# Kernel tuning notes

Hardware: AMD Instinct MI355X
Metric: run time of the kernel (lower is better)

Reference implementation:

```python
import jax, jax.numpy as jnp
import numpy as np

B_, L_, DIN, DM, DS, DR, K = 2, 1024, 1024, 2048, 16, 128, 4


def setup_inputs() -> dict:
    key = jax.random.key(0)
    ks = jax.random.split(key, 10)
    s = lambda k, shape, sc=0.02: (jax.random.normal(k, shape, jnp.float32) * sc)
    A_init = jnp.tile(jnp.arange(1, DS + 1, dtype=jnp.float32)[None, :], (DM, 1))  # (DM, DS)
    return {
        'x_in': jax.random.normal(ks[0], (B_, L_, DIN), jnp.float32),
        'W_in': s(ks[1], (DIN, DM)),
        'W_res': s(ks[2], (DIN, DM)),
        'W_out': s(ks[3], (DM, DIN)),
        'conv_w': s(ks[4], (DM, K), 0.1),   # depthwise conv weight (torch shape (DM,1,K) squeezed)
        'conv_b': jnp.zeros((DM,), jnp.float32),
        'A_log': jnp.log(A_init),
        'D': jnp.ones((DM,), jnp.float32),
        'W_B': s(ks[5], (DM, DS)),
        'W_C': s(ks[6], (DM, DS)),
        'W_dt': s(ks[7], (DM, DR)),
        'dt_w': s(ks[8], (DR, DM)),
        'dt_b': jnp.zeros((DM,), jnp.float32),
    }


def reference(x_in, W_in, W_res, W_out, conv_w, conv_b, A_log, D, W_B, W_C, W_dt, dt_w, dt_b):
    Bb, L, _ = x_in.shape
    x = x_in @ W_in                     # (B, L, DM)
    res = x_in @ W_res                  # (B, L, DM)
    # Causal depthwise conv1d: pad left k-1, truncate to L (matches Conv1d(padding=k-1)[:, :, :L])
    xp = jnp.pad(x, ((0, 0), (K - 1, 0), (0, 0)))
    xc = conv_b
    for i in range(K):
        xc = xc + xp[:, i:i + L, :] * conv_w[:, i]
    xc = jax.nn.silu(xc)                # (B, L, DM)
    # Selective SSM (fused_ssm)
    A = -jnp.exp(A_log)                 # (DM, DS)
    Bp = xc @ W_B                       # (B, L, DS)
    Cp = xc @ W_C                       # (B, L, DS)
    delta = jax.nn.softplus((xc @ W_dt) @ dt_w + dt_b)  # (B, L, DM)
    dA = jnp.exp(delta[..., None] * A)                       # (B, L, DM, DS)
    dBu = delta[..., None] * Bp[:, :, None, :] * xc[..., None]  # (B, L, DM, DS)

    def step(h, inp):
        dA_t, dBu_t, C_t = inp
        h = dA_t * h + dBu_t                         # (B, DM, DS)
        y = jnp.einsum('bdn,bn->bd', h, C_t)         # (B, DM)
        return h, y

    h0 = jnp.zeros((Bb, DM, DS), jnp.float32)
    _, ys = jax.lax.scan(step, h0, (dA.transpose(1, 0, 2, 3), dBu.transpose(1, 0, 2, 3), Cp.transpose(1, 0, 2)))
    y = ys.transpose(1, 0, 2) + D * xc  # (B, L, DM)
    y = y * jax.nn.silu(res)
    return y @ W_out                    # (B, L, DIN)
```

## Files before the change

### kernel.cpp

```cpp
#include <hip/hip_runtime.h>
#include <hip/hip_bf16.h>

constexpr int B_  = 2;
constexpr int L_  = 1024;
constexpr int DIN = 1024;
constexpr int DM  = 2048;
constexpr int DS  = 16;
constexpr int DR  = 128;
constexpr int KC  = 4;
constexpr int M_  = B_ * L_;
constexpr int NP2 = 256;
constexpr int NPC = 160;
constexpr int KSLICES = 8;
constexpr int KSL = DM / KSLICES;

constexpr int NC = 32;
constexpr int CL = L_ / NC;
constexpr int S_ = B_ * DM * DS;

typedef __bf16 bf16x8 __attribute__((ext_vector_type(8)));
typedef float  f32x4  __attribute__((ext_vector_type(4)));

__device__ __forceinline__ void gload_lds16(const void* g, void* l) {
    __builtin_amdgcn_global_load_lds(
        (const __attribute__((address_space(1))) void*)g,
        (__attribute__((address_space(3))) void*)l, 16, 0, 0);
}

__device__ __forceinline__ void transpose_block(const float* __restrict__ in,
                                                __bf16* __restrict__ out,
                                                int R, int C, int bx, int by, int t) {
    __shared__ float tile[32][33];
    int tx = t & 31, ty = t >> 5;
    #pragma unroll
    for (int j = 0; j < 32; j += 8)
        tile[ty + j][tx] = in[(size_t)(by * 32 + ty + j) * C + (bx * 32 + tx)];
    __syncthreads();
    #pragma unroll
    for (int j = 0; j < 32; j += 8)
        out[(size_t)(bx * 32 + ty + j) * R + (by * 32 + tx)] = (__bf16)tile[tx][ty + j];
}

__global__ void prep_all(const float* __restrict__ x_in, const float* __restrict__ W_in,
                         const float* __restrict__ W_res, const float* __restrict__ W_out,
                         const float* __restrict__ dt_w,
                         const float* __restrict__ W_B, const float* __restrict__ W_C,
                         const float* __restrict__ W_dt, const float* __restrict__ conv_w,
                         __bf16* __restrict__ xinB, __bf16* __restrict__ WinT,
                         __bf16* __restrict__ WresT, __bf16* __restrict__ WoutT,
                         __bf16* __restrict__ dtwT, __bf16* __restrict__ projW,
                         float* __restrict__ cwT) {
    int blk = blockIdx.x, t = threadIdx.x;
    if (blk < 8192) {
        int i = blk * 256 + t;
        xinB[i] = (__bf16)x_in[i];
    } else if (blk < 10240) {
        int b = blk - 8192;
        transpose_block(W_in, WinT, DIN, DM, b % 64, b / 64, t);
    } else if (blk < 12288) {
        int b = blk - 10240;
        transpose_block(W_res, WresT, DIN, DM, b % 64, b / 64, t);
    } else if (blk < 14336) {
        int b = blk - 12288;
        transpose_block(W_out, WoutT, DM, DIN, b % 32, b / 32, t);
    } else if (blk < 14592) {
        int b = blk - 14336;
        transpose_block(dt_w, dtwT, DR, DM, b % 64, b / 64, t);
    } else if (blk < 16640) {
        int i = (blk - 14592) * 256 + t;
        int k = i % DM;
        int n = i / DM;
        float v = 0.f;
        if (n < 16)        v = W_B[(size_t)k * DS + n];
        else if (n < 32)   v = W_C[(size_t)k * DS + (n - 16)];
        else if (n < 160)  v = W_dt[(size_t)k * DR + (n - 32)];
        projW[i] = (__bf16)v;
    } else {
        int j = (blk - 16640) * 256 + t;
        int tap = j / DM, d = j % DM;
        cwT[j] = conv_w[d * KC + tap];
    }
}

__global__ void reduce_split(const __bf16* __restrict__ PpartB, float* __restrict__ Bp,
                             float* __restrict__ Cp, __bf16* __restrict__ dtmpB) {
    int i = blockIdx.x * 256 + threadIdx.x;
    int row = i / NPC, c = i % NPC;
    float v = 0.f;
    #pragma unroll
    for (int ks = 0; ks < KSLICES; ks++)
        v += (float)PpartB[(size_t)ks * M_ * NPC + i];
    if (c < 16)       Bp[(size_t)row * DS + c] = v;
    else if (c < 32)  Cp[(size_t)row * DS + (c - 16)] = v;
    else              dtmpB[(size_t)row * DR + (c - 32)] = (__bf16)v;
}

template<int EPI>
__global__ void gemm_tile128(const __bf16* __restrict__ A, const __bf16* __restrict__ BT,
                             float* __restrict__ Cf, __bf16* __restrict__ Cb,
                             const float* __restrict__ bias, int M, int N, int K,
                             int lda, int ldb) {
    __shared__ __bf16 sA[2][128 * 32];
    __shared__ __bf16 sB[2][128 * 32];
    int t = threadIdx.x;
    int lane = t & 63, w = t >> 6;
    int wm = w >> 1, wn = w & 1;
    int m0 = blockIdx.y * 128, n0 = blockIdx.x * 128;
    int kbase = blockIdx.z * K;
    int q = lane >> 4, rr = lane & 15;

    f32x4 acc[4][4] = {};

    int srow = t >> 2;
    int slot = t & 3;

    const int nt = K >> 5;

    #pragma unroll
    for (int rnd = 0; rnd < 2; rnd++) {
        int row = srow + rnd * 64;
        int gkb = slot ^ ((row >> 1) & 3);
        gload_lds16(A  + (size_t)(m0 + row) * lda + kbase + gkb * 8,
                    &sA[0][rnd * 2048 + w * 512]);
        gload_lds16(BT + (size_t)(n0 + row) * ldb + kbase + gkb * 8,
                    &sB[0][rnd * 2048 + w * 512]);
    }
    __syncthreads();

    int cur = 0;
    for (int tix = 0; tix < nt; tix++) {
        if (tix + 1 < nt) {
            int kt = (tix + 1) << 5;
            #pragma unroll
            for (int rnd = 0; rnd < 2; rnd++) {
                int row = srow + rnd * 64;
                int gkb = slot ^ ((row >> 1) & 3);
                gload_lds16(A  + (size_t)(m0 + row) * lda + kbase + kt + gkb * 8,
                            &sA[cur ^ 1][rnd * 2048 + w * 512]);
                gload_lds16(BT + (size_t)(n0 + row) * ldb + kbase + kt + gkb * 8,
                            &sB[cur ^ 1][rnd * 2048 + w * 512]);
            }
        }

        bf16x8 af[4], bfr[4];
        #pragma unroll
        for (int i = 0; i < 4; i++) {
            int rowA = wm * 64 + i * 16 + rr;
            af[i] = *(const bf16x8*)(&sA[cur][rowA * 32 + ((q ^ ((rowA >> 1) & 3)) * 8)]);
            int rowB = wn * 64 + i * 16 + rr;
            bfr[i] = *(const bf16x8*)(&sB[cur][rowB * 32 + ((q ^ ((rowB >> 1) & 3)) * 8)]);
        }
        #pragma unroll
        for (int i = 0; i < 4; i++)
            #pragma unroll
            for (int j = 0; j < 4; j++)
                acc[i][j] = __builtin_amdgcn_mfma_f32_16x16x32_bf16(af[i], bfr[j], acc[i][j], 0, 0, 0);

        __syncthreads();
        cur ^= 1;
    }

    #pragma unroll
    for (int i = 0; i < 4; i++) {
        #pragma unroll
        for (int j = 0; j < 4; j++) {
            int col = n0 + wn * 64 + j * 16 + rr;
            #pragma unroll
            for (int jj = 0; jj < 4; jj++) {
                int row = m0 + wm * 64 + i * 16 + q * 4 + jj;
                float v = acc[i][j][jj];
                if (EPI == 1) {
                    float z = v + bias[col];
                    Cb[(size_t)row * N + col] = (__bf16)((z > 20.f) ? z : log1pf(__expf(z)));
                } else if (EPI == 2) {
                    if (col < DM) ((__bf16*)Cf)[(size_t)row * DM + col] = (__bf16)v;
                    else          Cb[(size_t)row * DM + (col - DM)] = (__bf16)v;
                } else {
                    if (col < NPC)
                        Cb[(size_t)blockIdx.z * M * NPC + (size_t)row * NPC + col] = (__bf16)v;
                }
            }
        }
    }
}

__global__ void gemm_out64(const __bf16* __restrict__ A, const __bf16* __restrict__ BT,
                           float* __restrict__ C, int M, int N, int K, int lda, int ldb) {
    __shared__ __bf16 sA[2][128 * 32];
    __shared__ __bf16 sB[2][64 * 32];
    int t = threadIdx.x;
    int lane = t & 63, w = t >> 6;
    int m0 = blockIdx.y * 128, n0 = blockIdx.x * 64;
    int q = lane >> 4, rr = lane & 15;

    f32x4 acc[2][4] = {};
    int srow = t >> 2;
    int slot = t & 3;

    const int nt = K >> 5;

    {
        #pragma unroll
        for (int rnd = 0; rnd < 2; rnd++) {
            int row = srow + rnd * 64;
            int gkb = slot ^ ((row >> 1) & 3);
            gload_lds16(A + (size_t)(m0 + row) * lda + gkb * 8,
                        &sA[0][rnd * 2048 + w * 512]);
        }
        int gkb = slot ^ ((srow >> 1) & 3);
        gload_lds16(BT + (size_t)(n0 + srow) * ldb + gkb * 8,
                    &sB[0][w * 512]);
    }
    __syncthreads();

    int cur = 0;
    for (int tix = 0; tix < nt; tix++) {
        if (tix + 1 < nt) {
            int kt = (tix + 1) << 5;
            #pragma unroll
            for (int rnd = 0; rnd < 2; rnd++) {
                int row = srow + rnd * 64;
                int gkb = slot ^ ((row >> 1) & 3);
                gload_lds16(A + (size_t)(m0 + row) * lda + kt + gkb * 8,
                            &sA[cur ^ 1][rnd * 2048 + w * 512]);
            }
            int gkb = slot ^ ((srow >> 1) & 3);
            gload_lds16(BT + (size_t)(n0 + srow) * ldb + kt + gkb * 8,
                        &sB[cur ^ 1][w * 512]);
        }

        bf16x8 af[2], bfr[4];
        #pragma unroll
        for (int i = 0; i < 2; i++) {
            int rowA = w * 32 + i * 16 + rr;
            af[i] = *(const bf16x8*)(&sA[cur][rowA * 32 + ((q ^ ((rowA >> 1) & 3)) * 8)]);
        }
        #pragma unroll
        for (int j = 0; j < 4; j++) {
            int rowB = j * 16 + rr;
            bfr[j] = *(const bf16x8*)(&sB[cur][rowB * 32 + ((q ^ ((rowB >> 1) & 3)) * 8)]);
        }
        #pragma unroll
        for (int i = 0; i < 2; i++)
            #pragma unroll
            for (int j = 0; j < 4; j++)
                acc[i][j] = __builtin_amdgcn_mfma_f32_16x16x32_bf16(af[i], bfr[j], acc[i][j], 0, 0, 0);

        __syncthreads();
        cur ^= 1;
    }

    #pragma unroll
    for (int i = 0; i < 2; i++) {
        #pragma unroll
        for (int j = 0; j < 4; j++) {
            int col = n0 + j * 16 + rr;
            #pragma unroll
            for (int jj = 0; jj < 4; jj++) {
                int row = m0 + w * 32 + i * 16 + q * 4 + jj;
                C[(size_t)row * N + col] = acc[i][j][jj];
            }
        }
    }
}

__global__ void conv_silu(const __bf16* __restrict__ x, const float* __restrict__ cwT,
                          const float* __restrict__ bias, __bf16* __restrict__ xcB) {
    int row = blockIdx.x;
    int d   = threadIdx.x * 8;
    int l   = row % L_;
    size_t base = (size_t)row * DM + d;

    float acc[8];
    {
        const f32x4* b4 = (const f32x4*)(bias + d);
        f32x4 b0 = b4[0], b1 = b4[1];
        #pragma unroll
        for (int q = 0; q < 4; q++) { acc[q] = b0[q]; acc[4 + q] = b1[q]; }
    }
    #pragma unroll
    for (int i = 0; i < KC; i++) {
        int li = l - (KC - 1) + i;
        if (li >= 0) {
            bf16x8 xv = *(const bf16x8*)(x + base + (size_t)(i - (KC - 1)) * DM);
            const f32x4* w4 = (const f32x4*)(cwT + (size_t)i * DM + d);
            f32x4 w0 = w4[0], w1 = w4[1];
            #pragma unroll
            for (int q = 0; q < 4; q++) {
                acc[q]     = fmaf((float)xv[q],     w0[q], acc[q]);
                acc[4 + q] = fmaf((float)xv[4 + q], w1[q], acc[4 + q]);
            }
        }
    }
    bf16x8 out;
    #pragma unroll
    for (int q = 0; q < 8; q++) {
        float v = acc[q] / (1.f + __expf(-acc[q]));
        out[q] = (__bf16)v;
    }
    *(bf16x8*)(xcB + base) = out;
}

__global__ void scan_phase1(const __bf16* __restrict__ delta, const __bf16* __restrict__ xc,
                            const float* __restrict__ Bp, const float* __restrict__ A_log,
                            __bf16* __restrict__ aprodB, __bf16* __restrict__ cendB) {
    int blk = blockIdx.x;
    int c   = blk % NC;
    int rem = blk / NC;
    int dmt = rem % (DM / 256);
    int b   = rem / (DM / 256);
    int t   = threadIdx.x;
    int dm  = dmt * 256 + t;
    int l0  = c * CL;

    __shared__ float sB[CL * DS];
    sB[t]       = Bp[((size_t)b * L_ + l0) * DS + t];
    sB[t + 256] = Bp[((size_t)b * L_ + l0) * DS + t + 256];
    __syncthreads();

    float Aval[DS];
    {
        const f32x4* Ap = (const f32x4*)(A_log + (size_t)dm * DS);
        #pragma unroll
        for (int r4 = 0; r4 < 4; r4++) {
            f32x4 a = Ap[r4];
            #pragma unroll
            for (int q = 0; q < 4; q++) Aval[r4 * 4 + q] = -__expf(a[q]);
        }
    }

    float h[DS], ap[DS];
    #pragma unroll
    for (int i = 0; i < DS; i++) { h[i] = 0.f; ap[i] = 1.f; }

    size_t base = ((size_t)b * L_ + l0) * DM + dm;
    #pragma unroll 4
    for (int j = 0; j < CL; j++) {
        float dl  = (float)delta[base + (size_t)j * DM];
        float xv  = (float)xc[base + (size_t)j * DM];
        float cmn = dl * xv;
        const f32x4* sB4 = (const f32x4*)(sB + j * DS);
        #pragma unroll
        for (int r4 = 0; r4 < 4; r4++) {
            f32x4 bv = sB4[r4];
            #pragma unroll
            for (int q = 0; q < 4; q++) {
                int i = r4 * 4 + q;
                float dA = __expf(dl * Aval[i]);
                ap[i] *= dA;
                h[i] = fmaf(dA, h[i], cmn * bv[q]);
            }
        }
    }

    size_t s = ((size_t)(b * DM + dm)) * DS;
    #pragma unroll
    for (int r8 = 0; r8 < 2; r8++) {
        bf16x8 va, vh;
        #pragma unroll
        for (int q = 0; q < 8; q++) { va[q] = (__bf16)ap[r8 * 8 + q]; vh[q] = (__bf16)h[r8 * 8 + q]; }
        ((bf16x8*)(aprodB + (size_t)c * S_ + s))[r8] = va;
        ((bf16x8*)(cendB  + (size_t)c * S_ + s))[r8] = vh;
    }
}

__global__ void scan_phase2(const __bf16* __restrict__ aprodB, const __bf16* __restrict__ cendB,
                            __bf16* __restrict__ hinitB) {
    int u = blockIdx.x * 256 + threadIdx.x;
    float h = 0.f;
    #pragma unroll
    for (int c = 0; c < NC; c++) {
        float a  = (float)aprodB[(size_t)c * S_ + u];
        float ce = (float)cendB [(size_t)c * S_ + u];
        hinitB[(size_t)c * S_ + u] = (__bf16)h;
        h = fmaf(a, h, ce);
    }
}

__global__ void scan_phase3(const __bf16* __restrict__ delta, const __bf16* __restrict__ xc,
                            const float* __restrict__ Bp, const float* __restrict__ Cp,
                            const __bf16* __restrict__ res, const float* __restrict__ A_log,
                            const float* __restrict__ Dw, const __bf16* __restrict__ hinitB,
                            __bf16* __restrict__ ybar) {
    int blk = blockIdx.x;
    int c   = blk % NC;
    int rem = blk / NC;
    int dmt = rem % (DM / 256);
    int b   = rem / (DM / 256);
    int t   = threadIdx.x;
    int dm  = dmt * 256 + t;
    int l0  = c * CL;

    __shared__ float sB[CL * DS];
    __shared__ float sC[CL * DS];
    sB[t]       = Bp[((size_t)b * L_ + l0) * DS + t];
    sB[t + 256] = Bp[((size_t)b * L_ + l0) * DS + t + 256];
    sC[t]       = Cp[((size_t)b * L_ + l0) * DS + t];
    sC[t + 256] = Cp[((size_t)b * L_ + l0) * DS + t + 256];
    __syncthreads();

    float Aval[DS];
    {
        const f32x4* Ap = (const f32x4*)(A_log + (size_t)dm * DS);
        #pragma unroll
        for (int r4 = 0; r4 < 4; r4++) {
            f32x4 a = Ap[r4];
            #pragma unroll
            for (int q = 0; q < 4; q++) Aval[r4 * 4 + q] = -__expf(a[q]);
        }
    }
    float Dval = Dw[dm];

    float h[DS];
    {
        size_t s = ((size_t)(b * DM + dm)) * DS;
        #pragma unroll
        for (int r8 = 0; r8 < 2; r8++) {
            bf16x8 v = ((const bf16x8*)(hinitB + (size_t)c * S_ + s))[r8];
            #pragma unroll
            for (int q = 0; q < 8; q++) h[r8 * 8 + q] = (float)v[q];
        }
    }

    size_t base = ((size_t)b * L_ + l0) * DM + dm;
    #pragma unroll 4
    for (int j = 0; j < CL; j++) {
        float dl  = (float)delta[base + (size_t)j * DM];
        float xv  = (float)xc[base + (size_t)j * DM];
        float rv  = (float)res[base + (size_t)j * DM];
        float cmn = dl * xv;
        float y = 0.f;
        const f32x4* sB4 = (const f32x4*)(sB + j * DS);
        const f32x4* sC4 = (const f32x4*)(sC + j * DS);
        #pragma unroll
        for (int r4 = 0; r4 < 4; r4++) {
            f32x4 bv = sB4[r4];
            f32x4 cv = sC4[r4];
            #pragma unroll
            for (int q = 0; q < 4; q++) {
                int i = r4 * 4 + q;
                float dA = __expf(dl * Aval[i]);
                h[i] = fmaf(dA, h[i], cmn * bv[q]);
                y = fmaf(h[i], cv[q], y);
            }
        }
        float g = rv / (1.f + __expf(-rv));
        ybar[base + (size_t)j * DM] = (__bf16)((y + Dval * xv) * g);
    }
}

extern "C" void kernel_launch(void* const* d_in, const int* in_sizes, int n_in,
                              void* d_out, int out_size, void* d_ws, size_t ws_size,
                              hipStream_t stream) {
    const float* x_in   = (const float*)d_in[0];
    const float* W_in   = (const float*)d_in[1];
    const float* W_res  = (const float*)d_in[2];
    const float* W_out  = (const float*)d_in[3];
    const float* conv_w = (const float*)d_in[4];
    const float* conv_b = (const float*)d_in[5];
    const float* A_log  = (const float*)d_in[6];
    const float* Dw     = (const float*)d_in[7];
    const float* W_B    = (const float*)d_in[8];
    const float* W_C    = (const float*)d_in[9];
    const float* W_dt   = (const float*)d_in[10];
    const float* dt_w   = (const float*)d_in[11];
    const float* dt_b   = (const float*)d_in[12];

    float* ws_f = (float*)d_ws;
    float* Bp    = ws_f;
    float* Cp    = Bp + (size_t)M_ * DS;
    float* cwT   = Cp + (size_t)M_ * DS;
    __bf16* bf_base = (__bf16*)(cwT + (size_t)KC * DM);
    __bf16* ybar   = bf_base;
    __bf16* xinB   = ybar   + (size_t)M_ * DM;
    __bf16* WinT   = xinB   + (size_t)M_ * DIN;
    __bf16* WresT  = WinT   + (size_t)DM * DIN;
    __bf16* WoutT  = WresT  + (size_t)DM * DIN;
    __bf16* xB     = WoutT  + (size_t)DIN * DM;
    __bf16* xcB    = xB     + (size_t)M_ * DM;
    __bf16* projW  = xcB    + (size_t)M_ * DM;
    __bf16* dtwT   = projW  + (size_t)NP2 * DM;
    __bf16* dtmpB  = dtwT   + (size_t)DM * DR;
    __bf16* deltaB = dtmpB  + (size_t)M_ * DR;
    __bf16* resB   = deltaB + (size_t)M_ * DM;
    __bf16* aprodB = resB   + (size_t)M_ * DM;
    __bf16* cendB  = aprodB + (size_t)NC * S_;
    __bf16* hinitB = cendB  + (size_t)NC * S_;
    __bf16* PpartB = hinitB + (size_t)NC * S_;

    prep_all<<<16672, 256, 0, stream>>>(x_in, W_in, W_res, W_out, dt_w, W_B, W_C, W_dt,
                                        conv_w, xinB, WinT, WresT, WoutT, dtwT, projW, cwT);

    gemm_tile128<2><<<dim3((2 * DM) / 128, M_ / 128, 1), 256, 0, stream>>>(
        xinB, WinT, (float*)xB, resB, nullptr, M_, 2 * DM, DIN, DIN, DIN);

    conv_silu<<<M_, 256, 0, stream>>>(xB, cwT, conv_b, xcB);

    gemm_tile128<4><<<dim3(NP2 / 128, M_ / 128, KSLICES), 256, 0, stream>>>(
        xcB, projW, nullptr, PpartB, nullptr, M_, NP2, KSL, DM, DM);
    reduce_split<<<(M_ * NPC) / 256, 256, 0, stream>>>(PpartB, Bp, Cp, dtmpB);

    gemm_tile128<1><<<dim3(DM / 128, M_ / 128, 1), 256, 0, stream>>>(
        dtmpB, dtwT, nullptr, deltaB, dt_b, M_, DM, DR, DR, DR);

    int nblk = B_ * (DM / 256) * NC;
    scan_phase1<<<nblk, 256, 0, stream>>>(deltaB, xcB, Bp, A_log, aprodB, cendB);
    scan_phase2<<<S_ / 256, 256, 0, stream>>>(aprodB, cendB, hinitB);
    scan_phase3<<<nblk, 256, 0, stream>>>(deltaB, xcB, Bp, Cp, resB, A_log, Dw, hinitB, ybar);

    gemm_out64<<<dim3(DIN / 64, M_ / 128), 256, 0, stream>>>(
        ybar, WoutT, (float*)d_out, M_, DIN, DM, DM, DM);
}
```

Measured before the change: 263.3 us.

## Triple-buffer GEMM LDS tiles with explicit vmcnt waits and raw barriers

Both bf16 GEMM kernels move from double to triple buffering of the LDS tiles. Two tiles are prefetched ahead via global_load_lds, and each wait uses explicit s_waitcnt vmcnt counts with raw s_barrier instead of __syncthreads. The aim is to hide more global-load latency behind the MFMA work. In exchange LDS use grows by half, which may lower occupancy. The hand-counted vmcnt values are fragile if the compiler issues other vector memory ops, and raw barriers do not wait on LDS reads the way __syncthreads does.

```diff
diff --git a/kernel.cpp b/kernel.cpp
--- a/kernel.cpp
+++ b/kernel.cpp
@@ -26,6 +26,8 @@
         (const __attribute__((address_space(1))) void*)g,
         (__attribute__((address_space(3))) void*)l, 16, 0, 0);
 }
+
+#define VMCNT(N) asm volatile("s_waitcnt vmcnt(" #N ")" ::: "memory")
 
 __device__ __forceinline__ void transpose_block(const float* __restrict__ in,
                                                 __bf16* __restrict__ out,
@@ -100,8 +102,8 @@
                              float* __restrict__ Cf, __bf16* __restrict__ Cb,
                              const float* __restrict__ bias, int M, int N, int K,
                              int lda, int ldb) {
-    __shared__ __bf16 sA[2][128 * 32];
-    __shared__ __bf16 sB[2][128 * 32];
+    __shared__ __bf16 sA[3][128 * 32];
+    __shared__ __bf16 sB[3][128 * 32];
     int t = threadIdx.x;
     int lane = t & 63, w = t >> 6;
     int wm = w >> 1, wn = w & 1;
@@ -116,32 +118,29 @@
 
     const int nt = K >> 5;
 
-    #pragma unroll
-    for (int rnd = 0; rnd < 2; rnd++) {
-        int row = srow + rnd * 64;
-        int gkb = slot ^ ((row >> 1) & 3);
-        gload_lds16(A  + (size_t)(m0 + row) * lda + kbase + gkb * 8,
-                    &sA[0][rnd * 2048 + w * 512]);
-        gload_lds16(BT + (size_t)(n0 + row) * ldb + kbase + gkb * 8,
-                    &sB[0][rnd * 2048 + w * 512]);
-    }
-    __syncthreads();
+    auto stage = [&](int tile, int bufi) {
+        int kt = tile << 5;
+        #pragma unroll
+        for (int rnd = 0; rnd < 2; rnd++) {
+            int row = srow + rnd * 64;
+            int gkb = slot ^ ((row >> 1) & 3);
+            gload_lds16(A  + (size_t)(m0 + row) * lda + kbase + kt + gkb * 8,
+                        &sA[bufi][rnd * 2048 + w * 512]);
+            gload_lds16(BT + (size_t)(n0 + row) * ldb + kbase + kt + gkb * 8,
+                        &sB[bufi][rnd * 2048 + w * 512]);
+        }
+    };
+
+    if (0 < nt) stage(0, 0);
+    if (1 < nt) stage(1, 1);
+    if (2 < nt) stage(2, 2);
+    if (nt >= 3)      { VMCNT(8); }
+    else if (nt == 2) { VMCNT(4); }
+    else              { VMCNT(0); }
+    __builtin_amdgcn_s_barrier();
 
     int cur = 0;
     for (int tix = 0; tix < nt; tix++) {
-        if (tix + 1 < nt) {
-            int kt = (tix + 1) << 5;
-            #pragma unroll
-            for (int rnd = 0; rnd < 2; rnd++) {
-                int row = srow + rnd * 64;
-                int gkb = slot ^ ((row >> 1) & 3);
-                gload_lds16(A  + (size_t)(m0 + row) * lda + kbase + kt + gkb * 8,
-                            &sA[cur ^ 1][rnd * 2048 + w * 512]);
-                gload_lds16(BT + (size_t)(n0 + row) * ldb + kbase + kt + gkb * 8,
-                            &sB[cur ^ 1][rnd * 2048 + w * 512]);
-            }
-        }
-
         bf16x8 af[4], bfr[4];
         #pragma unroll
         for (int i = 0; i < 4; i++) {
@@ -156,8 +155,16 @@
             for (int j = 0; j < 4; j++)
                 acc[i][j] = __builtin_amdgcn_mfma_f32_16x16x32_bf16(af[i], bfr[j], acc[i][j], 0, 0, 0);
 
-        __syncthreads();
-        cur ^= 1;
+        __builtin_amdgcn_s_barrier();
+        if (tix + 3 < nt) stage(tix + 3, cur);
+        int rem = nt - 1 - tix;
+        if (rem > 0) {
+            if (rem >= 3)      { VMCNT(8); }
+            else if (rem == 2) { VMCNT(4); }
+            else               { VMCNT(0); }
+            __builtin_amdgcn_s_barrier();
+        }
+        cur = (cur == 2) ? 0 : cur + 1;
     }
 
     #pragma unroll
@@ -186,8 +193,8 @@
 
 __global__ void gemm_out64(const __bf16* __restrict__ A, const __bf16* __restrict__ BT,
                            float* __restrict__ C, int M, int N, int K, int lda, int ldb) {
-    __shared__ __bf16 sA[2][128 * 32];
-    __shared__ __bf16 sB[2][64 * 32];
+    __shared__ __bf16 sA[3][128 * 32];
+    __shared__ __bf16 sB[3][64 * 32];
     int t = threadIdx.x;
     int lane = t & 63, w = t >> 6;
     int m0 = blockIdx.y * 128, n0 = blockIdx.x * 64;
@@ -199,36 +206,30 @@
 
     const int nt = K >> 5;
 
-    {
+    auto stage = [&](int tile, int bufi) {
+        int kt = tile << 5;
         #pragma unroll
         for (int rnd = 0; rnd < 2; rnd++) {
             int row = srow + rnd * 64;
             int gkb = slot ^ ((row >> 1) & 3);
-            gload_lds16(A + (size_t)(m0 + row) * lda + gkb * 8,
-                        &sA[0][rnd * 2048 + w * 512]);
+            gload_lds16(A + (size_t)(m0 + row) * lda + kt + gkb * 8,
+                        &sA[bufi][rnd * 2048 + w * 512]);
         }
         int gkb = slot ^ ((srow >> 1) & 3);
-        gload_lds16(BT + (size_t)(n0 + srow) * ldb + gkb * 8,
-                    &sB[0][w * 512]);
-    }
-    __syncthreads();
+        gload_lds16(BT + (size_t)(n0 + srow) * ldb + kt + gkb * 8,
+                    &sB[bufi][w * 512]);
+    };
+
+    if (0 < nt) stage(0, 0);
+    if (1 < nt) stage(1, 1);
+    if (2 < nt) stage(2, 2);
+    if (nt >= 3)      { VMCNT(6); }
+    else if (nt == 2) { VMCNT(3); }
+    else              { VMCNT(0); }
+    __builtin_amdgcn_s_barrier();
 
     int cur = 0;
     for (int tix = 0; tix < nt; tix++) {
-        if (tix + 1 < nt) {
-            int kt = (tix + 1) << 5;
-            #pragma unroll
-            for (int rnd = 0; rnd < 2; rnd++) {
-                int row = srow + rnd * 64;
-                int gkb = slot ^ ((row >> 1) & 3);
-                gload_lds16(A + (size_t)(m0 + row) * lda + kt + gkb * 8,
-                            &sA[cur ^ 1][rnd * 2048 + w * 512]);
-            }
-            int gkb = slot ^ ((srow >> 1) & 3);
-            gload_lds16(BT + (size_t)(n0 + srow) * ldb + kt + gkb * 8,
-                        &sB[cur ^ 1][w * 512]);
-        }
-
         bf16x8 af[2], bfr[4];
         #pragma unroll
         for (int i = 0; i < 2; i++) {
@@ -246,8 +247,16 @@
             for (int j = 0; j < 4; j++)
                 acc[i][j] = __builtin_amdgcn_mfma_f32_16x16x32_bf16(af[i], bfr[j], acc[i][j], 0, 0, 0);
 
-        __syncthreads();
-        cur ^= 1;
+        __builtin_amdgcn_s_barrier();
+        if (tix + 3 < nt) stage(tix + 3, cur);
+        int rem = nt - 1 - tix;
+        if (rem > 0) {
+            if (rem >= 3)      { VMCNT(6); }
+            else if (rem == 2) { VMCNT(3); }
+            else               { VMCNT(0); }
+            __builtin_amdgcn_s_barrier();
+        }
+        cur = (cur == 2) ? 0 : cur + 1;
     }
 
     #pragma unroll
```

After: 375.1 us. 42.4% more time.

## Use 8 waves per block in GEMM kernels with smaller per-wave subtiles

Applied to the files above, without the earlier changes.

All bf16 MFMA GEMM kernels are launched with 512 threads instead of 256. The block tile stays the same, but each wave now owns half as many output fragments: 64x32 instead of 64x64 in the 128x128 kernel, and 32x32 instead of 32x64 in the output GEMM. The LDS staging is restructured so each thread issues one async global-to-LDS load per matrix per k-step, and the B load in the 64-wide kernel is guarded to threads below 256. The aim is more waves per CU for latency hiding and fewer accumulator registers per thread. In exchange, each wave reuses fragments less, which means more LDS reads per MFMA, and larger blocks add barrier cost.

```diff
diff --git a/kernel.cpp b/kernel.cpp
--- a/kernel.cpp
+++ b/kernel.cpp
@@ -104,56 +104,48 @@
     __shared__ __bf16 sB[2][128 * 32];
     int t = threadIdx.x;
     int lane = t & 63, w = t >> 6;
-    int wm = w >> 1, wn = w & 1;
+    int wm = w >> 2, wn = w & 3;
     int m0 = blockIdx.y * 128, n0 = blockIdx.x * 128;
     int kbase = blockIdx.z * K;
     int q = lane >> 4, rr = lane & 15;
 
-    f32x4 acc[4][4] = {};
+    f32x4 acc[4][2] = {};
 
     int srow = t >> 2;
     int slot = t & 3;
 
     const int nt = K >> 5;
 
-    #pragma unroll
-    for (int rnd = 0; rnd < 2; rnd++) {
-        int row = srow + rnd * 64;
-        int gkb = slot ^ ((row >> 1) & 3);
-        gload_lds16(A  + (size_t)(m0 + row) * lda + kbase + gkb * 8,
-                    &sA[0][rnd * 2048 + w * 512]);
-        gload_lds16(BT + (size_t)(n0 + row) * ldb + kbase + gkb * 8,
-                    &sB[0][rnd * 2048 + w * 512]);
-    }
+    auto stage = [&](int kt, int bufi) {
+        int gkb = slot ^ ((srow >> 1) & 3);
+        gload_lds16(A  + (size_t)(m0 + srow) * lda + kbase + kt + gkb * 8,
+                    &sA[bufi][w * 512]);
+        gload_lds16(BT + (size_t)(n0 + srow) * ldb + kbase + kt + gkb * 8,
+                    &sB[bufi][w * 512]);
+    };
+
+    stage(0, 0);
     __syncthreads();
 
     int cur = 0;
     for (int tix = 0; tix < nt; tix++) {
-        if (tix + 1 < nt) {
-            int kt = (tix + 1) << 5;
-            #pragma unroll
-            for (int rnd = 0; rnd < 2; rnd++) {
-                int row = srow + rnd * 64;
-                int gkb = slot ^ ((row >> 1) & 3);
-                gload_lds16(A  + (size_t)(m0 + row) * lda + kbase + kt + gkb * 8,
-                            &sA[cur ^ 1][rnd * 2048 + w * 512]);
-                gload_lds16(BT + (size_t)(n0 + row) * ldb + kbase + kt + gkb * 8,
-                            &sB[cur ^ 1][rnd * 2048 + w * 512]);
-            }
-        }
-
-        bf16x8 af[4], bfr[4];
+        if (tix + 1 < nt) stage((tix + 1) << 5, cur ^ 1);
+
+        bf16x8 af[4], bfr[2];
         #pragma unroll
         for (int i = 0; i < 4; i++) {
             int rowA = wm * 64 + i * 16 + rr;
             af[i] = *(const bf16x8*)(&sA[cur][rowA * 32 + ((q ^ ((rowA >> 1) & 3)) * 8)]);
-            int rowB = wn * 64 + i * 16 + rr;
-            bfr[i] = *(const bf16x8*)(&sB[cur][rowB * 32 + ((q ^ ((rowB >> 1) & 3)) * 8)]);
+        }
+        #pragma unroll
+        for (int j = 0; j < 2; j++) {
+            int rowB = wn * 32 + j * 16 + rr;
+            bfr[j] = *(const bf16x8*)(&sB[cur][rowB * 32 + ((q ^ ((rowB >> 1) & 3)) * 8)]);
         }
         #pragma unroll
         for (int i = 0; i < 4; i++)
             #pragma unroll
-            for (int j = 0; j < 4; j++)
+            for (int j = 0; j < 2; j++)
                 acc[i][j] = __builtin_amdgcn_mfma_f32_16x16x32_bf16(af[i], bfr[j], acc[i][j], 0, 0, 0);
 
         __syncthreads();
@@ -163,8 +155,8 @@
     #pragma unroll
     for (int i = 0; i < 4; i++) {
         #pragma unroll
-        for (int j = 0; j < 4; j++) {
-            int col = n0 + wn * 64 + j * 16 + rr;
+        for (int j = 0; j < 2; j++) {
+            int col = n0 + wn * 32 + j * 16 + rr;
             #pragma unroll
             for (int jj = 0; jj < 4; jj++) {
                 int row = m0 + wm * 64 + i * 16 + q * 4 + jj;
@@ -190,60 +182,47 @@
     __shared__ __bf16 sB[2][64 * 32];
     int t = threadIdx.x;
     int lane = t & 63, w = t >> 6;
+    int wm = w >> 1, wn = w & 1;
     int m0 = blockIdx.y * 128, n0 = blockIdx.x * 64;
     int q = lane >> 4, rr = lane & 15;
 
-    f32x4 acc[2][4] = {};
+    f32x4 acc[2][2] = {};
     int srow = t >> 2;
     int slot = t & 3;
 
     const int nt = K >> 5;
 
-    {
-        #pragma unroll
-        for (int rnd = 0; rnd < 2; rnd++) {
-            int row = srow + rnd * 64;
-            int gkb = slot ^ ((row >> 1) & 3);
-            gload_lds16(A + (size_t)(m0 + row) * lda + gkb * 8,
-                        &sA[0][rnd * 2048 + w * 512]);
-        }
+    auto stage = [&](int kt, int bufi) {
         int gkb = slot ^ ((srow >> 1) & 3);
-        gload_lds16(BT + (size_t)(n0 + srow) * ldb + gkb * 8,
-                    &sB[0][w * 512]);
-    }
+        gload_lds16(A + (size_t)(m0 + srow) * lda + kt + gkb * 8,
+                    &sA[bufi][w * 512]);
+        if (t < 256)
+            gload_lds16(BT + (size_t)(n0 + srow) * ldb + kt + gkb * 8,
+                        &sB[bufi][w * 512]);
+    };
+
+    stage(0, 0);
     __syncthreads();
 
     int cur = 0;
     for (int tix = 0; tix < nt; tix++) {
-        if (tix + 1 < nt) {
-            int kt = (tix + 1) << 5;
-            #pragma unroll
-            for (int rnd = 0; rnd < 2; rnd++) {
-                int row = srow + rnd * 64;
-                int gkb = slot ^ ((row >> 1) & 3);
-                gload_lds16(A + (size_t)(m0 + row) * lda + kt + gkb * 8,
-                            &sA[cur ^ 1][rnd * 2048 + w * 512]);
-            }
-            int gkb = slot ^ ((srow >> 1) & 3);
-            gload_lds16(BT + (size_t)(n0 + srow) * ldb + kt + gkb * 8,
-                        &sB[cur ^ 1][w * 512]);
-        }
-
-        bf16x8 af[2], bfr[4];
+        if (tix + 1 < nt) stage((tix + 1) << 5, cur ^ 1);
+
+        bf16x8 af[2], bfr[2];
         #pragma unroll
         for (int i = 0; i < 2; i++) {
-            int rowA = w * 32 + i * 16 + rr;
+            int rowA = wm * 32 + i * 16 + rr;
             af[i] = *(const bf16x8*)(&sA[cur][rowA * 32 + ((q ^ ((rowA >> 1) & 3)) * 8)]);
         }
         #pragma unroll
-        for (int j = 0; j < 4; j++) {
-            int rowB = j * 16 + rr;
+        for (int j = 0; j < 2; j++) {
+            int rowB = wn * 32 + j * 16 + rr;
             bfr[j] = *(const bf16x8*)(&sB[cur][rowB * 32 + ((q ^ ((rowB >> 1) & 3)) * 8)]);
         }
         #pragma unroll
         for (int i = 0; i < 2; i++)
             #pragma unroll
-            for (int j = 0; j < 4; j++)
+            for (int j = 0; j < 2; j++)
                 acc[i][j] = __builtin_amdgcn_mfma_f32_16x16x32_bf16(af[i], bfr[j], acc[i][j], 0, 0, 0);
 
         __syncthreads();
@@ -253,11 +232,11 @@
     #pragma unroll
     for (int i = 0; i < 2; i++) {
         #pragma unroll
-        for (int j = 0; j < 4; j++) {
-            int col = n0 + j * 16 + rr;
+        for (int j = 0; j < 2; j++) {
+            int col = n0 + wn * 32 + j * 16 + rr;
             #pragma unroll
             for (int jj = 0; jj < 4; jj++) {
-                int row = m0 + w * 32 + i * 16 + q * 4 + jj;
+                int row = m0 + wm * 32 + i * 16 + q * 4 + jj;
                 C[(size_t)row * N + col] = acc[i][j][jj];
             }
         }
@@ -491,16 +470,16 @@
     prep_all<<<16672, 256, 0, stream>>>(x_in, W_in, W_res, W_out, dt_w, W_B, W_C, W_dt,
                                         conv_w, xinB, WinT, WresT, WoutT, dtwT, projW, cwT);
 
-    gemm_tile128<2><<<dim3((2 * DM) / 128, M_ / 128, 1), 256, 0, stream>>>(
+    gemm_tile128<2><<<dim3((2 * DM) / 128, M_ / 128, 1), 512, 0, stream>>>(
         xinB, WinT, (float*)xB, resB, nullptr, M_, 2 * DM, DIN, DIN, DIN);
 
     conv_silu<<<M_, 256, 0, stream>>>(xB, cwT, conv_b, xcB);
 
-    gemm_tile128<4><<<dim3(NP2 / 128, M_ / 128, KSLICES), 256, 0, stream>>>(
+    gemm_tile128<4><<<dim3(NP2 / 128, M_ / 128, KSLICES), 512, 0, stream>>>(
         xcB, projW, nullptr, PpartB, nullptr, M_, NP2, KSL, DM, DM);
     reduce_split<<<(M_ * NPC) / 256, 256, 0, stream>>>(PpartB, Bp, Cp, dtmpB);
 
-    gemm_tile128<1><<<dim3(DM / 128, M_ / 128, 1), 256, 0, stream>>>(
+    gemm_tile128<1><<<dim3(DM / 128, M_ / 128, 1), 512, 0, stream>>>(
         dtmpB, dtwT, nullptr, deltaB, dt_b, M_, DM, DR, DR, DR);
 
     int nblk = B_ * (DM / 256) * NC;
@@ -508,6 +487,6 @@
     scan_phase2<<<S_ / 256, 256, 0, stream>>>(aprodB, cendB, hinitB);
     scan_phase3<<<nblk, 256, 0, stream>>>(deltaB, xcB, Bp, Cp, resB, A_log, Dw, hinitB, ybar);
 
-    gemm_out64<<<dim3(DIN / 64, M_ / 128), 256, 0, stream>>>(
+    gemm_out64<<<dim3(DIN / 64, M_ / 128), 512, 0, stream>>>(
         ybar, WoutT, (float*)d_out, M_, DIN, DM, DM, DM);
 }
```

After: 249.2 us. 5.4% less time.
